# Kernel optimization log

Measured on AMD Instinct MI355X. Metric: run time of the kernel, lower is better.

Reference implementation:

```python
import jax, jax.numpy as jnp
import numpy as np

B, S, D, V = 2, 2048, 1024, 32000
EPS_LN = 1e-5
EPS_BN = 1e-5


def setup_inputs() -> dict:
    key = jax.random.key(0)
    ks = jax.random.split(key, 8)
    s = lambda k, shape: jax.random.normal(k, shape, jnp.float32) * 0.02
    return dict(
        X=jax.random.randint(ks[0], (B, S), 0, V, dtype=jnp.int32),
        emb=s(ks[1], (V, D)),
        w_hg=s(ks[2], (D, 2 * D)),            # minGRU to_hidden_and_gate (bias-free)
        conv_w=s(ks[3], (D, D, 3)),           # Conv1d OIW
        conv_b=jnp.zeros((D,), jnp.float32),
        bn_g=jnp.ones((D,), jnp.float32), bn_b=jnp.zeros((D,), jnp.float32),
        ln_g=jnp.ones((D,), jnp.float32), ln_b=jnp.zeros((D,), jnp.float32),
        w1=s(ks[4], (D, 2 * D)), b1=jnp.zeros((2 * D,), jnp.float32),
        w2=s(ks[5], (2 * D, 2 * D)), b2=jnp.zeros((2 * D,), jnp.float32),
        w3=s(ks[6], (2 * D, V)), b3=jnp.zeros((V,), jnp.float32),
    )


def _log_g(x):
    # log of g(x) = where(x>=0, x+0.5, sigmoid(x))
    return jnp.where(x >= 0, jnp.log(jax.nn.relu(x) + 0.5), -jax.nn.softplus(-x))


def _min_gru(x, w_hg):
    # Heinsen log-space associative scan (lucidrains minGRU, expansion=1)
    hg = x @ w_hg                              # [B,S,2D]
    hidden, gate = jnp.split(hg, 2, axis=-1)
    log_coeffs = -jax.nn.softplus(gate)        # log(1 - z)
    log_values = -jax.nn.softplus(-gate) + _log_g(hidden)  # log z + log h~
    a_star = jnp.cumsum(log_coeffs, axis=1)
    log_h = a_star + jax.lax.cumlogsumexp(log_values - a_star, axis=1)
    return jnp.exp(log_h)                      # [B,S,D]


def reference(X, emb, w_hg, conv_w, conv_b, bn_g, bn_b, ln_g, ln_b,
              w1, b1, w2, b2, w3, b3):
    x = emb[X]                                 # [B,S,D]
    shortcut = x
    h = _min_gru(x, w_hg)                      # dropout rate 0 -> identity
    mu = jnp.mean(h, axis=-1, keepdims=True)
    var = jnp.mean((h - mu) ** 2, axis=-1, keepdims=True)
    h = (h - mu) / jnp.sqrt(var + EPS_LN) * ln_g + ln_b
    x = h + shortcut
    xc = jnp.transpose(x, (0, 2, 1))           # [B,D,S]
    xc = jax.lax.conv_general_dilated(
        xc, conv_w, window_strides=(1,), padding=[(1, 1)],
        dimension_numbers=('NCW', 'OIW', 'NCW')) + conv_b[None, :, None]
    m = jnp.mean(xc, axis=(0, 2), keepdims=True)       # BN training-mode stats
    v = jnp.mean((xc - m) ** 2, axis=(0, 2), keepdims=True)
    xc = (xc - m) / jnp.sqrt(v + EPS_BN) * bn_g[None, :, None] + bn_b[None, :, None]
    x = jnp.transpose(xc, (0, 2, 1))           # [B,S,D]
    x = jax.nn.relu(x @ w1 + b1)
    x = jax.nn.relu(x @ w2 + b2)
    return x @ w3 + b3                         # [B,S,V]
```

## Files before the change

### kernel.cpp

```cpp
#include <hip/hip_runtime.h>
#include <hip/hip_bf16.h>

#define B_  2
#define S_  2048
#define D_  1024
#define V_  32000
#define BS_ 4096

typedef __attribute__((ext_vector_type(4))) float f32x4;
typedef __attribute__((ext_vector_type(8))) short short8;
typedef unsigned long long u64;
typedef unsigned short u16;

__device__ __forceinline__ u16 f2bf(float x) {
  unsigned int u = __float_as_uint(x);
  u += 0x7FFFu + ((u >> 16) & 1u);
  return (u16)(u >> 16);
}
__device__ __forceinline__ u64 pack4bf(float a, float b, float c, float d) {
  return (u64)f2bf(a) | ((u64)f2bf(b) << 16) | ((u64)f2bf(c) << 32) | ((u64)f2bf(d) << 48);
}

#define GLOAD_LDS16(g, l) __builtin_amdgcn_global_load_lds( \
    (const __attribute__((address_space(1))) void*)(g),     \
    (__attribute__((address_space(3))) void*)(l), 16, 0, 0)

__device__ __forceinline__ unsigned lds_addr32(const void* p) {
  return (unsigned)(uintptr_t)(const __attribute__((address_space(3))) void*)p;
}
__device__ __forceinline__ short8 ds_read128(unsigned a) {
  short8 r;
  asm volatile("ds_read_b128 %0, %1" : "=&v"(r) : "v"(a));
  return r;
}

template<bool RELU, bool BF16OUT, bool HASBIAS>
__global__ __launch_bounds__(256) void gemm_bt(
    const u16* __restrict__ A, const u16* __restrict__ Bt,
    const float* __restrict__ bias, void* __restrict__ Cout,
    int M, int N, int K)
{
  __shared__ __attribute__((aligned(16))) u16 Alds[128 * 64];
  __shared__ __attribute__((aligned(16))) u16 Blds[128 * 64];
  const int tid = threadIdx.x;
  const int w = tid >> 6, l = tid & 63;
  const int wr = w >> 1, wc = w & 1;
  const int m0 = blockIdx.y * 128, n0 = blockIdx.x * 128;
  const int lr = l >> 3, lc = l & 7;
  const int fr = l & 15, fq = l >> 4;

  const u16* Ag = A + (size_t)(m0 + w * 8 + lr) * K + lc * 8;
  const u16* Bg = Bt + (size_t)(n0 + w * 8 + lr) * K + lc * 8;

  f32x4 acc[4][4];
#pragma unroll
  for (int i = 0; i < 4; ++i)
#pragma unroll
    for (int j = 0; j < 4; ++j) acc[i][j] = {0.f, 0.f, 0.f, 0.f};

  for (int kt = 0; kt < K; kt += 64) {
#pragma unroll
    for (int r = 0; r < 4; ++r) {
      GLOAD_LDS16(Ag + (size_t)(r * 32) * K + kt, &Alds[(r * 32 + w * 8) * 64]);
      GLOAD_LDS16(Bg + (size_t)(r * 32) * K + kt, &Blds[(r * 32 + w * 8) * 64]);
    }
    __syncthreads();
#pragma unroll
    for (int ks = 0; ks < 2; ++ks) {
      short8 af[4], bfv[4];
#pragma unroll
      for (int i = 0; i < 4; ++i)
        af[i] = *reinterpret_cast<const short8*>(
            &Alds[(wr * 64 + i * 16 + fr) * 64 + ks * 32 + fq * 8]);
#pragma unroll
      for (int j = 0; j < 4; ++j)
        bfv[j] = *reinterpret_cast<const short8*>(
            &Blds[(wc * 64 + j * 16 + fr) * 64 + ks * 32 + fq * 8]);
#pragma unroll
      for (int i = 0; i < 4; ++i)
#pragma unroll
        for (int j = 0; j < 4; ++j)
          acc[i][j] = __builtin_amdgcn_mfma_f32_16x16x32_bf16(af[i], bfv[j], acc[i][j], 0, 0, 0);
    }
    __syncthreads();
  }

  const int row0 = m0 + wr * 64 + fq * 4;
  const int col0 = n0 + wc * 64 + fr;
#pragma unroll
  for (int j = 0; j < 4; ++j) {
    const int col = col0 + j * 16;
    const float bv = HASBIAS ? bias[col] : 0.f;
#pragma unroll
    for (int i = 0; i < 4; ++i) {
#pragma unroll
      for (int r = 0; r < 4; ++r) {
        const int row = row0 + i * 16 + r;
        float v = acc[i][j][r] + bv;
        if (RELU) v = fmaxf(v, 0.f);
        if (BF16OUT) ((u16*)Cout)[(size_t)row * N + col] = f2bf(v);
        else         ((float*)Cout)[(size_t)row * N + col] = v;
      }
    }
  }
}

#define BARRIER() __builtin_amdgcn_s_barrier()
#define WAITL0_PIN() do { asm volatile("s_waitcnt lgkmcnt(0)" ::: "memory"); \
                          __builtin_amdgcn_sched_barrier(0); } while (0)
#define VMCNTN(n) asm volatile("s_waitcnt vmcnt(" #n ")" ::: "memory")

template<bool RELU, bool BF16OUT, bool HASBIAS>
__global__ __launch_bounds__(512, 2) void gemm256_bt(
    const u16* __restrict__ A, const u16* __restrict__ Bt,
    const float* __restrict__ bias, void* __restrict__ Cout,
    int M, int N, int K)
{
  __shared__ __attribute__((aligned(16))) u16 LDS[65536];
  const int tid = threadIdx.x;
  const int w = tid >> 6, l = tid & 63;
  const int wr = w >> 2, wc = w & 3;
  const int fr = l & 15, fq = l >> 4;
  const unsigned ldsb = lds_addr32(&LDS[0]);

  const int MTt = M >> 8;
  const int total = MTt * (N >> 8);
  const int perx = total >> 3;
  const int p = (blockIdx.x & 7) * perx + (blockIdx.x >> 3);
  const int m0 = (p % MTt) << 8;
  const int n0 = (p / MTt) << 8;

  const int NT = K >> 6;
  const u16* Abase = A + (size_t)m0 * K;
  const u16* Bbase = Bt + (size_t)n0 * K;

  const int rq_[2] = { w * 16 + (l >> 3), w * 16 + 8 + (l >> 3) };
  const int gq_[2] = { (l & 7) ^ (rq_[0] & 7), (l & 7) ^ (rq_[1] & 7) };
  const u16* gA[2][2];
  const u16* gB[2][2];
#pragma unroll
  for (int h = 0; h < 2; ++h)
#pragma unroll
    for (int q = 0; q < 2; ++q) {
      gA[h][q] = Abase + (size_t)(h * 128 + rq_[q]) * K + gq_[q] * 8;
      gB[h][q] = Bbase + (size_t)(h * 128 + rq_[q]) * K + gq_[q] * 8;
    }

  const int swz0 = ((0 * 4 + fq) ^ (fr & 7)) * 16;
  const int swz1 = ((1 * 4 + fq) ^ (fr & 7)) * 16;
  const unsigned aB = ldsb + 16384u * wr + 128u * fr;
  const unsigned bB = ldsb + 32768u + 16384u * (wc >> 1) + 128u * ((wc & 1) * 64 + fr);
  const unsigned bA00 = aB + swz0,           bA01 = aB + swz1;
  const unsigned bA10 = aB + 65536u + swz0,  bA11 = aB + 65536u + swz1;
  const unsigned bB00 = bB + swz0,           bB01 = bB + swz1;
  const unsigned bB10 = bB + 65536u + swz0,  bB11 = bB + 65536u + swz1;

#define STAGE_A(h, t, buf) do { _Pragma("unroll")                            \
  for (int q_ = 0; q_ < 2; ++q_)                                             \
    GLOAD_LDS16(gA[h][q_] + (size_t)(t) * 64,                                \
                &LDS[(((buf) * 4) + (h)) * 8192 + (w * 128 + q_ * 64) * 8]); \
} while (0)
#define STAGE_B(h, t, buf) do { _Pragma("unroll")                            \
  for (int q_ = 0; q_ < 2; ++q_)                                             \
    GLOAD_LDS16(gB[h][q_] + (size_t)(t) * 64,                                \
                &LDS[(((buf) * 4) + 2 + (h)) * 8192 + (w * 128 + q_ * 64) * 8]); \
} while (0)

#define RDA_(arr, k0, k1, Q) do { _Pragma("unroll")                          \
  for (int i_ = 0; i_ < 4; ++i_) {                                           \
    arr[i_][0] = ds_read128((k0) + (Q) * 8192 + i_ * 2048);                  \
    arr[i_][1] = ds_read128((k1) + (Q) * 8192 + i_ * 2048);                  \
  } } while (0)
#define RDB_(arr, k0, k1, JQ) do { _Pragma("unroll")                         \
  for (int j_ = 0; j_ < 2; ++j_) {                                           \
    arr[j_][0] = ds_read128((k0) + (JQ) * 4096 + j_ * 2048);                 \
    arr[j_][1] = ds_read128((k1) + (JQ) * 4096 + j_ * 2048);                 \
  } } while (0)

#define MFMA_Q(arrA, arrB, itb, jtb) do { _Pragma("unroll")                  \
  for (int i_ = 0; i_ < 4; ++i_)                                             \
    _Pragma("unroll")                                                        \
    for (int j_ = 0; j_ < 2; ++j_)                                           \
      _Pragma("unroll")                                                      \
      for (int ks_ = 0; ks_ < 2; ++ks_)                                      \
        acc[(itb) + i_][(jtb) + j_] = __builtin_amdgcn_mfma_f32_16x16x32_bf16( \
            arrA[i_][ks_], arrB[j_][ks_], acc[(itb) + i_][(jtb) + j_], 0, 0, 0); \
} while (0)

  f32x4 acc[8][4];
#pragma unroll
  for (int i = 0; i < 8; ++i)
#pragma unroll
    for (int j = 0; j < 4; ++j) acc[i][j] = {0.f, 0.f, 0.f, 0.f};

  short8 a0[4][2], a1[4][2], b0[2][2], b1[2][2];

  STAGE_A(0, 0, 0); STAGE_A(1, 0, 0); STAGE_B(0, 0, 0); STAGE_B(1, 0, 0);
  STAGE_B(0, 1, 1); STAGE_A(0, 1, 1);
  VMCNTN(4);
  BARRIER();

#define TILE(t, cb, nb) do {                                                 \
                                         \
  RDA_(a0, bA##cb##0, bA##cb##1, 0);                                         \
  RDB_(b0, bB##cb##0, bB##cb##1, 0);                                         \
  if ((t) + 1 < NT) STAGE_A(1, (t) + 1, nb);                                 \
  BARRIER(); WAITL0_PIN();                                                   \
  __builtin_amdgcn_s_setprio(1); MFMA_Q(a0, b0, 0, 0); __builtin_amdgcn_s_setprio(0); \
  BARRIER();                                                                 \
                                            \
  RDB_(b1, bB##cb##0, bB##cb##1, 1);                                         \
  if ((t) + 1 < NT) STAGE_B(1, (t) + 1, nb);                                 \
  BARRIER(); WAITL0_PIN();                                                   \
  __builtin_amdgcn_s_setprio(1); MFMA_Q(a0, b1, 0, 2); __builtin_amdgcn_s_setprio(0); \
  BARRIER();                                                                 \
                                            \
  RDA_(a1, bA##cb##0, bA##cb##1, 1);                                         \
  if ((t) + 2 < NT) STAGE_B(0, (t) + 2, cb);                                 \
  BARRIER(); WAITL0_PIN();                                                   \
  __builtin_amdgcn_s_setprio(1); MFMA_Q(a1, b1, 4, 2); __builtin_amdgcn_s_setprio(0); \
  BARRIER();                                                                 \
                     \
  if ((t) + 2 < NT) STAGE_A(0, (t) + 2, cb);                                 \
  BARRIER(); WAITL0_PIN();                                                   \
  __builtin_amdgcn_s_setprio(1); MFMA_Q(a1, b0, 4, 0); __builtin_amdgcn_s_setprio(0); \
  if ((t) + 2 < NT) { VMCNTN(4); } else { VMCNTN(0); }                       \
  BARRIER();                                                                 \
} while (0)

  for (int t = 0; t < NT; t += 2) {
    TILE(t, 0, 1);
    TILE(t + 1, 1, 0);
  }
#undef TILE

  float* lf = (float*)(void*)(&LDS[0]) + (size_t)w * 1056;
  const int row_base = m0 + wr * 128;
  const int col_base = n0 + wc * 64;
  float bvv[4];
#pragma unroll
  for (int jt = 0; jt < 4; ++jt)
    bvv[jt] = HASBIAS ? bias[col_base + jt * 16 + fr] : 0.f;
  const int er = l >> 4, ec = (l & 15) * 4;
#pragma unroll
  for (int it = 0; it < 8; ++it) {
#pragma unroll
    for (int jt = 0; jt < 4; ++jt)
#pragma unroll
      for (int rr = 0; rr < 4; ++rr)
        lf[(fq * 4 + rr) * 66 + jt * 16 + fr] = acc[it][jt][rr] + bvv[jt];
#pragma unroll
    for (int ch = 0; ch < 4; ++ch) {
      f32x4 vv = *(const f32x4*)&lf[(ch * 4 + er) * 66 + ec];
      if (RELU) {
        vv[0] = fmaxf(vv[0], 0.f); vv[1] = fmaxf(vv[1], 0.f);
        vv[2] = fmaxf(vv[2], 0.f); vv[3] = fmaxf(vv[3], 0.f);
      }
      const int grow = row_base + it * 16 + ch * 4 + er;
      if (BF16OUT) {
        *(u64*)(&((u16*)Cout)[(size_t)grow * N + col_base + ec]) =
            pack4bf(vv[0], vv[1], vv[2], vv[3]);
      } else {
        *(f32x4*)(&((float*)Cout)[(size_t)grow * N + col_base + ec]) = vv;
      }
    }
  }
#undef STAGE_A
#undef STAGE_B
#undef RDA_
#undef RDB_
#undef MFMA_Q
}

__global__ __launch_bounds__(256) void transpose_f2b(
    const float* __restrict__ in, u16* __restrict__ out, int K, int N)
{
  __shared__ float t[32][33];
  const int n0 = blockIdx.x * 32, k0 = blockIdx.y * 32;
  const int r = threadIdx.x >> 5, cc = threadIdx.x & 31;
#pragma unroll
  for (int rr = 0; rr < 4; ++rr) {
    const int ki = rr * 8 + r;
    t[ki][cc] = in[(size_t)(k0 + ki) * N + n0 + cc];
  }
  __syncthreads();
#pragma unroll
  for (int rr = 0; rr < 4; ++rr) {
    const int ni = rr * 8 + r;
    out[(size_t)(n0 + ni) * K + k0 + cc] = f2bf(t[cc][ni]);
  }
}

__global__ __launch_bounds__(256) void convw_reorder(
    const float* __restrict__ cw, u16* __restrict__ out)
{
  const int gid = blockIdx.x * 256 + threadIdx.x;
  const int o = gid >> 10, i = gid & 1023;
  const float w0 = cw[(size_t)gid * 3 + 0];
  const float w1 = cw[(size_t)gid * 3 + 1];
  const float w2 = cw[(size_t)gid * 3 + 2];
  out[(size_t)o * 3072 + i]          = f2bf(w0);
  out[(size_t)o * 3072 + 1024 + i]   = f2bf(w1);
  out[(size_t)o * 3072 + 2048 + i]   = f2bf(w2);
}

__global__ __launch_bounds__(256) void gather_emb(
    const int* __restrict__ X, const float* __restrict__ emb, u16* __restrict__ xb)
{
  const int row = blockIdx.x;
  const int tok = X[row];
  const int d4 = threadIdx.x * 4;
  const float4 v = *reinterpret_cast<const float4*>(emb + (size_t)tok * D_ + d4);
  *(u64*)(&xb[(size_t)row * D_ + d4]) = pack4bf(v.x, v.y, v.z, v.w);
}

#define GRU_CP(hid_, gate_, h_, cp_) {                                   \
  const float t_ = __expf(-(gate_));                                     \
  const float z_ = 1.f / (1.f + t_);                                     \
  const float c_ = t_ * z_;                                              \
  const float g_ = ((hid_) >= 0.f) ? ((hid_) + 0.5f)                     \
                                   : (1.f / (1.f + __expf(-(hid_))));    \
  (h_) = c_ * (h_) + z_ * g_; (cp_) *= c_; }

#define GRU_NC(hid_, gate_, h_) {                                        \
  const float t_ = __expf(-(gate_));                                     \
  const float z_ = 1.f / (1.f + t_);                                     \
  const float g_ = ((hid_) >= 0.f) ? ((hid_) + 0.5f)                     \
                                   : (1.f / (1.f + __expf(-(hid_))));    \
  (h_) = (t_ * z_) * (h_) + z_ * g_; }

__global__ __launch_bounds__(256) void scan_partial(
    const float* __restrict__ hg, float* __restrict__ Cb, float* __restrict__ Vb)
{
  const int b = blockIdx.x >> 6, c = blockIdx.x & 63;
  const int d4 = threadIdx.x * 4;
  const float* base = hg + ((size_t)b * S_ + (size_t)c * 32) * (2 * D_);
  float h[4] = {0.f, 0.f, 0.f, 0.f}, cp[4] = {1.f, 1.f, 1.f, 1.f};
  for (int t = 0; t < 32; ++t) {
    const float4 hd = *reinterpret_cast<const float4*>(base + (size_t)t * (2 * D_) + d4);
    const float4 gt = *reinterpret_cast<const float4*>(base + (size_t)t * (2 * D_) + D_ + d4);
    GRU_CP(hd.x, gt.x, h[0], cp[0]); GRU_CP(hd.y, gt.y, h[1], cp[1]);
    GRU_CP(hd.z, gt.z, h[2], cp[2]); GRU_CP(hd.w, gt.w, h[3], cp[3]);
  }
  const size_t o = ((size_t)(b * 64 + c)) * D_ + d4;
  *(float4*)(Cb + o) = make_float4(cp[0], cp[1], cp[2], cp[3]);
  *(float4*)(Vb + o) = make_float4(h[0], h[1], h[2], h[3]);
}

__global__ void scan_carry(const float* __restrict__ Cb, const float* __restrict__ Vb,
                           float* __restrict__ Hs)
{
  const int gid = blockIdx.x * 256 + threadIdx.x;
  const int b = gid >> 10, d = gid & 1023;
  float h = 0.f;
  for (int c = 0; c < 64; ++c) {
    const size_t o = ((size_t)(b * 64 + c)) * D_ + d;
    Hs[o] = h;
    h = Cb[o] * h + Vb[o];
  }
}

__global__ __launch_bounds__(256) void scan_emit(
    const float* __restrict__ hg, const float* __restrict__ Hs,
    const int* __restrict__ X, const float* __restrict__ emb,
    const float* __restrict__ ln_g, const float* __restrict__ ln_b,
    u16* __restrict__ Aconv)
{
  __shared__ float red[4];
  const int b = blockIdx.x >> 6, c = blockIdx.x & 63;
  const int tid = threadIdx.x;
  const int w = tid >> 6, l = tid & 63;
  const int d4 = tid * 4;
  const float* base = hg + ((size_t)b * S_ + (size_t)c * 32) * (2 * D_);
  float h0, h1, h2, h3;
  {
    const float4 hs = *reinterpret_cast<const float4*>(Hs + ((size_t)(b * 64 + c)) * D_ + d4);
    h0 = hs.x; h1 = hs.y; h2 = hs.z; h3 = hs.w;
  }
  const float4 lg = *reinterpret_cast<const float4*>(ln_g + d4);
  const float4 lb = *reinterpret_cast<const float4*>(ln_b + d4);

  for (int t = 0; t < 32; ++t) {
    const int s = c * 32 + t;
    const float4 hd = *reinterpret_cast<const float4*>(base + (size_t)t * (2 * D_) + d4);
    const float4 gt = *reinterpret_cast<const float4*>(base + (size_t)t * (2 * D_) + D_ + d4);
    GRU_NC(hd.x, gt.x, h0); GRU_NC(hd.y, gt.y, h1);
    GRU_NC(hd.z, gt.z, h2); GRU_NC(hd.w, gt.w, h3);

    float sm = h0 + h1 + h2 + h3;
#pragma unroll
    for (int m = 1; m < 64; m <<= 1) sm += __shfl_xor(sm, m);
    __syncthreads();
    if (l == 0) red[w] = sm;
    __syncthreads();
    const float mu = (red[0] + red[1] + red[2] + red[3]) * (1.f / (float)D_);
    float q = (h0 - mu) * (h0 - mu) + (h1 - mu) * (h1 - mu) +
              (h2 - mu) * (h2 - mu) + (h3 - mu) * (h3 - mu);
#pragma unroll
    for (int m = 1; m < 64; m <<= 1) q += __shfl_xor(q, m);
    __syncthreads();
    if (l == 0) red[w] = q;
    __syncthreads();
    const float var = (red[0] + red[1] + red[2] + red[3]) * (1.f / (float)D_);
    const float rstd = rsqrtf(var + 1e-5f);

    const int tok = X[b * S_ + s];
    const float4 e = *reinterpret_cast<const float4*>(emb + (size_t)tok * D_ + d4);
    const float x0 = (h0 - mu) * rstd * lg.x + lb.x + e.x;
    const float x1 = (h1 - mu) * rstd * lg.y + lb.y + e.y;
    const float x2 = (h2 - mu) * rstd * lg.z + lb.z + e.z;
    const float x3 = (h3 - mu) * rstd * lg.w + lb.w + e.w;
    const u64 pk = pack4bf(x0, x1, x2, x3);

    const size_t row = (size_t)b * S_ + s;
    *(u64*)(&Aconv[row * 3072 + D_ + d4]) = pk;
    if (s + 1 < S_) *(u64*)(&Aconv[(row + 1) * 3072 + d4]) = pk;
    if (s > 0)      *(u64*)(&Aconv[(row - 1) * 3072 + 2 * D_ + d4]) = pk;
    if (s == 0)       *(u64*)(&Aconv[row * 3072 + d4]) = 0ull;
    if (s == S_ - 1)  *(u64*)(&Aconv[row * 3072 + 2 * D_ + d4]) = 0ull;
  }
}

__global__ __launch_bounds__(256) void bn_partial(
    const float* __restrict__ cv, float* __restrict__ ps, float* __restrict__ pq)
{
  const int blk = blockIdx.x;
  const int c4 = threadIdx.x * 4;
  float s0 = 0, s1 = 0, s2 = 0, s3 = 0, q0 = 0, q1 = 0, q2 = 0, q3 = 0;
  for (int r = 0; r < 64; ++r) {
    const float4 v = *reinterpret_cast<const float4*>(cv + ((size_t)blk * 64 + r) * D_ + c4);
    s0 += v.x; s1 += v.y; s2 += v.z; s3 += v.w;
    q0 += v.x * v.x; q1 += v.y * v.y; q2 += v.z * v.z; q3 += v.w * v.w;
  }
  *(float4*)(ps + (size_t)blk * D_ + c4) = make_float4(s0, s1, s2, s3);
  *(float4*)(pq + (size_t)blk * D_ + c4) = make_float4(q0, q1, q2, q3);
}

__global__ void bn_finalize(const float* __restrict__ ps, const float* __restrict__ pq,
                            const float* __restrict__ bn_g, const float* __restrict__ bn_b,
                            float* __restrict__ scale, float* __restrict__ shift)
{
  const int c = blockIdx.x * 256 + threadIdx.x;
  float s = 0.f, q = 0.f;
  for (int blk = 0; blk < 64; ++blk) { s += ps[(size_t)blk * D_ + c]; q += pq[(size_t)blk * D_ + c]; }
  const float m = s * (1.f / (float)BS_);
  const float var = q * (1.f / (float)BS_) - m * m;
  const float rs = rsqrtf(var + 1e-5f);
  const float sc = bn_g[c] * rs;
  scale[c] = sc;
  shift[c] = bn_b[c] - m * sc;
}

__global__ __launch_bounds__(256) void bn_apply(
    const float* __restrict__ cv, const float* __restrict__ scale,
    const float* __restrict__ shift, u16* __restrict__ out)
{
  const size_t idx = ((size_t)blockIdx.x * 256 + threadIdx.x) * 4;
  const int c = (int)(idx & 1023);
  const float4 v = *reinterpret_cast<const float4*>(cv + idx);
  const float4 sc = *reinterpret_cast<const float4*>(scale + c);
  const float4 sh = *reinterpret_cast<const float4*>(shift + c);
  *(u64*)(&out[idx]) = pack4bf(v.x * sc.x + sh.x, v.y * sc.y + sh.y,
                               v.z * sc.z + sh.z, v.w * sc.w + sh.w);
}

extern "C" void kernel_launch(void* const* d_in, const int* in_sizes, int n_in,
                              void* d_out, int out_size, void* d_ws, size_t ws_size,
                              hipStream_t stream)
{
  const int*   X      = (const int*)d_in[0];
  const float* emb    = (const float*)d_in[1];
  const float* w_hg   = (const float*)d_in[2];
  const float* conv_w = (const float*)d_in[3];
  const float* bn_g   = (const float*)d_in[5];
  const float* bn_b   = (const float*)d_in[6];
  const float* ln_g   = (const float*)d_in[7];
  const float* ln_b   = (const float*)d_in[8];
  const float* w1     = (const float*)d_in[9];
  const float* b1     = (const float*)d_in[10];
  const float* w2     = (const float*)d_in[11];
  const float* b2     = (const float*)d_in[12];
  const float* w3     = (const float*)d_in[13];
  const float* b3     = (const float*)d_in[14];
  float* out = (float*)d_out;
  char* ws = (char*)d_ws;

  const size_t OFF_A4    = 0;
  const size_t BASE      = 16777216;
  const size_t OFF_W3T   = BASE;
  const size_t OFF_WHGT  = BASE;
  const size_t OFF_W1T   = BASE + 4194304;
  const size_t OFF_W2T   = OFF_W1T + 4194304;
  const size_t OFF_WCVT  = OFF_W2T + 8388608;
  const size_t OFF_XBF   = OFF_WCVT + 6291456;
  const size_t OFF_HG    = OFF_XBF + 8388608;
  const size_t OFF_CB    = OFF_HG + 33554432;
  const size_t OFF_VB    = OFF_CB + 524288;
  const size_t OFF_HS    = OFF_VB + 524288;
  const size_t OFF_ACONV = OFF_HS + 524288;
  const size_t OFF_CVO   = OFF_ACONV + 25165824;
  const size_t OFF_A2    = OFF_CVO + 16777216;
  const size_t OFF_A3    = OFF_A2 + 8388608;
  const size_t OFF_BNS   = OFF_A3 + 16777216;
  const size_t OFF_BNQ   = OFF_BNS + 262144;
  const size_t OFF_SC    = OFF_BNQ + 262144;
  const size_t OFF_SH    = OFF_SC + 4096;
  (void)in_sizes; (void)n_in; (void)out_size; (void)ws_size;

  u16*   WHGT = (u16*)(ws + OFF_WHGT);
  u16*   W1T  = (u16*)(ws + OFF_W1T);
  u16*   W2T  = (u16*)(ws + OFF_W2T);
  u16*   W3T  = (u16*)(ws + OFF_W3T);
  u16*   WCVT = (u16*)(ws + OFF_WCVT);
  u16*   XBF  = (u16*)(ws + OFF_XBF);
  float* HG   = (float*)(ws + OFF_HG);
  float* CB   = (float*)(ws + OFF_CB);
  float* VB   = (float*)(ws + OFF_VB);
  float* HS   = (float*)(ws + OFF_HS);
  u16*   ACONV= (u16*)(ws + OFF_ACONV);
  float* CVO  = (float*)(ws + OFF_CVO);
  u16*   A2   = (u16*)(ws + OFF_A2);
  u16*   A3   = (u16*)(ws + OFF_A3);
  u16*   A4   = (u16*)(ws + OFF_A4);
  float* BNS  = (float*)(ws + OFF_BNS);
  float* BNQ  = (float*)(ws + OFF_BNQ);
  float* SC   = (float*)(ws + OFF_SC);
  float* SH   = (float*)(ws + OFF_SH);

  transpose_f2b<<<dim3(2048 / 32, 1024 / 32), 256, 0, stream>>>(w_hg, WHGT, 1024, 2048);
  transpose_f2b<<<dim3(2048 / 32, 1024 / 32), 256, 0, stream>>>(w1,   W1T,  1024, 2048);
  transpose_f2b<<<dim3(2048 / 32, 2048 / 32), 256, 0, stream>>>(w2,   W2T,  2048, 2048);
  convw_reorder<<<4096, 256, 0, stream>>>(conv_w, WCVT);

  gather_emb<<<BS_, 256, 0, stream>>>(X, emb, XBF);

  gemm_bt<false, false, false><<<dim3(2048 / 128, BS_ / 128), 256, 0, stream>>>(
      XBF, WHGT, nullptr, HG, BS_, 2048, 1024);

  scan_partial<<<B_ * 64, 256, 0, stream>>>(HG, CB, VB);
  scan_carry<<<8, 256, 0, stream>>>(CB, VB, HS);
  scan_emit<<<B_ * 64, 256, 0, stream>>>(HG, HS, X, emb, ln_g, ln_b, ACONV);

  gemm_bt<false, false, false><<<dim3(1024 / 128, BS_ / 128), 256, 0, stream>>>(
      ACONV, WCVT, nullptr, CVO, BS_, 1024, 3072);

  bn_partial<<<64, 256, 0, stream>>>(CVO, BNS, BNQ);
  bn_finalize<<<4, 256, 0, stream>>>(BNS, BNQ, bn_g, bn_b, SC, SH);
  bn_apply<<<4096, 256, 0, stream>>>(CVO, SC, SH, A2);

  gemm_bt<true, true, true><<<dim3(2048 / 128, BS_ / 128), 256, 0, stream>>>(
      A2, W1T, b1, A3, BS_, 2048, 1024);
  gemm_bt<true, true, true><<<dim3(2048 / 128, BS_ / 128), 256, 0, stream>>>(
      A3, W2T, b2, A4, BS_, 2048, 2048);

  transpose_f2b<<<dim3(V_ / 32, 2048 / 32), 256, 0, stream>>>(w3, W3T, 2048, V_);
  gemm256_bt<false, false, true><<<dim3((BS_ / 256) * (V_ / 256)), 512, 0, stream>>>(
      A4, W3T, b3, out, BS_, V_, 2048);
}
```

Baseline: 915.1 us.

## Switch vocab GEMM to 32x32x16 MFMA and chunked column-major tile order

```diff
diff --git a/kernel.cpp b/kernel.cpp
--- a/kernel.cpp
+++ b/kernel.cpp
@@ -8,6 +8,7 @@
 #define BS_ 4096
 
 typedef __attribute__((ext_vector_type(4))) float f32x4;
+typedef __attribute__((ext_vector_type(16))) float f32x16;
 typedef __attribute__((ext_vector_type(8))) short short8;
 typedef unsigned long long u64;
 typedef unsigned short u16;
@@ -27,11 +28,6 @@
 
 __device__ __forceinline__ unsigned lds_addr32(const void* p) {
   return (unsigned)(uintptr_t)(const __attribute__((address_space(3))) void*)p;
-}
-__device__ __forceinline__ short8 ds_read128(unsigned a) {
-  short8 r;
-  asm volatile("ds_read_b128 %0, %1" : "=&v"(r) : "v"(a));
-  return r;
 }
 
 template<bool RELU, bool BF16OUT, bool HASBIAS>
@@ -109,26 +105,27 @@
 #define WAITL0_PIN() do { asm volatile("s_waitcnt lgkmcnt(0)" ::: "memory"); \
                           __builtin_amdgcn_sched_barrier(0); } while (0)
 #define VMCNTN(n) asm volatile("s_waitcnt vmcnt(" #n ")" ::: "memory")
+#define DSR(dst, base, imm) \
+  asm volatile("ds_read_b128 %0, %1 offset:" #imm : "=&v"(dst) : "v"(base))
 
 template<bool RELU, bool BF16OUT, bool HASBIAS>
 __global__ __launch_bounds__(512, 2) void gemm256_bt(
     const u16* __restrict__ A, const u16* __restrict__ Bt,
     const float* __restrict__ bias, void* __restrict__ Cout,
-    int M, int N, int K)
+    int M, int N, int K, int CW)
 {
   __shared__ __attribute__((aligned(16))) u16 LDS[65536];
   const int tid = threadIdx.x;
   const int w = tid >> 6, l = tid & 63;
   const int wr = w >> 2, wc = w & 3;
-  const int fr = l & 15, fq = l >> 4;
+  const int hi = l >> 5, lo = l & 31;
   const unsigned ldsb = lds_addr32(&LDS[0]);
 
   const int MTt = M >> 8;
-  const int total = MTt * (N >> 8);
-  const int perx = total >> 3;
-  const int p = (blockIdx.x & 7) * perx + (blockIdx.x >> 3);
-  const int m0 = (p % MTt) << 8;
-  const int n0 = (p / MTt) << 8;
+  const int bpc = MTt * CW;
+  const int chunk = blockIdx.x / bpc, rem = blockIdx.x % bpc;
+  const int m0 = (rem % MTt) << 8;
+  const int n0 = ((chunk * CW) + rem / MTt) << 8;
 
   const int NT = K >> 6;
   const u16* Abase = A + (size_t)m0 * K;
@@ -146,14 +143,21 @@
       gB[h][q] = Bbase + (size_t)(h * 128 + rq_[q]) * K + gq_[q] * 8;
     }
 
-  const int swz0 = ((0 * 4 + fq) ^ (fr & 7)) * 16;
-  const int swz1 = ((1 * 4 + fq) ^ (fr & 7)) * 16;
-  const unsigned aB = ldsb + 16384u * wr + 128u * fr;
-  const unsigned bB = ldsb + 32768u + 16384u * (wc >> 1) + 128u * ((wc & 1) * 64 + fr);
-  const unsigned bA00 = aB + swz0,           bA01 = aB + swz1;
-  const unsigned bA10 = aB + 65536u + swz0,  bA11 = aB + 65536u + swz1;
-  const unsigned bB00 = bB + swz0,           bB01 = bB + swz1;
-  const unsigned bB10 = bB + 65536u + swz0,  bB11 = bB + 65536u + swz1;
+  unsigned swz[4];
+#pragma unroll
+  for (int s = 0; s < 4; ++s)
+    swz[s] = (unsigned)((((s * 2 + hi) ^ (l & 7))) * 16);
+  const unsigned baseA = ldsb + wr * 16384u + (unsigned)lo * 128u;
+  const unsigned baseB = ldsb + 32768u + (wc >> 1) * 16384u +
+                         (unsigned)((wc & 1) * 64 + lo) * 128u;
+  const unsigned bA00 = baseA + swz[0], bA01 = baseA + swz[1];
+  const unsigned bA02 = baseA + swz[2], bA03 = baseA + swz[3];
+  const unsigned bA10 = bA00 + 65536u, bA11 = bA01 + 65536u;
+  const unsigned bA12 = bA02 + 65536u, bA13 = bA03 + 65536u;
+  const unsigned bB00 = baseB + swz[0], bB01 = baseB + swz[1];
+  const unsigned bB02 = baseB + swz[2], bB03 = baseB + swz[3];
+  const unsigned bB10 = bB00 + 65536u, bB11 = bB01 + 65536u;
+  const unsigned bB12 = bB02 + 65536u, bB13 = bB03 + 65536u;
 
 #define STAGE_A(h, t, buf) do { _Pragma("unroll")                            \
   for (int q_ = 0; q_ < 2; ++q_)                                             \
@@ -166,34 +170,23 @@
                 &LDS[(((buf) * 4) + 2 + (h)) * 8192 + (w * 128 + q_ * 64) * 8]); \
 } while (0)
 
-#define RDA_(arr, k0, k1, Q) do { _Pragma("unroll")                          \
-  for (int i_ = 0; i_ < 4; ++i_) {                                           \
-    arr[i_][0] = ds_read128((k0) + (Q) * 8192 + i_ * 2048);                  \
-    arr[i_][1] = ds_read128((k1) + (Q) * 8192 + i_ * 2048);                  \
-  } } while (0)
-#define RDB_(arr, k0, k1, JQ) do { _Pragma("unroll")                         \
-  for (int j_ = 0; j_ < 2; ++j_) {                                           \
-    arr[j_][0] = ds_read128((k0) + (JQ) * 4096 + j_ * 2048);                 \
-    arr[j_][1] = ds_read128((k1) + (JQ) * 4096 + j_ * 2048);                 \
-  } } while (0)
-
-#define MFMA_Q(arrA, arrB, itb, jtb) do { _Pragma("unroll")                  \
-  for (int i_ = 0; i_ < 4; ++i_)                                             \
+#define MMQ2(IB, J, arrA, arrB) do { _Pragma("unroll")                       \
+  for (int ii_ = 0; ii_ < 2; ++ii_)                                          \
     _Pragma("unroll")                                                        \
-    for (int j_ = 0; j_ < 2; ++j_)                                           \
-      _Pragma("unroll")                                                      \
-      for (int ks_ = 0; ks_ < 2; ++ks_)                                      \
-        acc[(itb) + i_][(jtb) + j_] = __builtin_amdgcn_mfma_f32_16x16x32_bf16( \
-            arrA[i_][ks_], arrB[j_][ks_], acc[(itb) + i_][(jtb) + j_], 0, 0, 0); \
+    for (int s_ = 0; s_ < 4; ++s_)                                           \
+      acc[(IB) + ii_][J] = __builtin_amdgcn_mfma_f32_32x32x16_bf16(          \
+          arrA[ii_][s_], arrB[s_], acc[(IB) + ii_][J], 0, 0, 0);             \
 } while (0)
 
-  f32x4 acc[8][4];
-#pragma unroll
-  for (int i = 0; i < 8; ++i)
-#pragma unroll
-    for (int j = 0; j < 4; ++j) acc[i][j] = {0.f, 0.f, 0.f, 0.f};
-
-  short8 a0[4][2], a1[4][2], b0[2][2], b1[2][2];
+  f32x16 acc[4][2];
+#pragma unroll
+  for (int i = 0; i < 4; ++i)
+#pragma unroll
+    for (int j = 0; j < 2; ++j)
+#pragma unroll
+      for (int e = 0; e < 16; ++e) acc[i][j][e] = 0.f;
+
+  short8 a01[2][4], a23[2][4], b0[4], b1[4];
 
   STAGE_A(0, 0, 0); STAGE_A(1, 0, 0); STAGE_B(0, 0, 0); STAGE_B(1, 0, 0);
   STAGE_B(0, 1, 1); STAGE_A(0, 1, 1);
@@ -201,29 +194,37 @@
   BARRIER();
 
 #define TILE(t, cb, nb) do {                                                 \
-                                         \
-  RDA_(a0, bA##cb##0, bA##cb##1, 0);                                         \
-  RDB_(b0, bB##cb##0, bB##cb##1, 0);                                         \
+           \
+  DSR(a01[0][0], bA##cb##0, 0);    DSR(a01[0][1], bA##cb##1, 0);             \
+  DSR(a01[0][2], bA##cb##2, 0);    DSR(a01[0][3], bA##cb##3, 0);             \
+  DSR(a01[1][0], bA##cb##0, 4096); DSR(a01[1][1], bA##cb##1, 4096);          \
+  DSR(a01[1][2], bA##cb##2, 4096); DSR(a01[1][3], bA##cb##3, 4096);          \
+  DSR(b0[0], bB##cb##0, 0); DSR(b0[1], bB##cb##1, 0);                        \
+  DSR(b0[2], bB##cb##2, 0); DSR(b0[3], bB##cb##3, 0);                        \
   if ((t) + 1 < NT) STAGE_A(1, (t) + 1, nb);                                 \
   BARRIER(); WAITL0_PIN();                                                   \
-  __builtin_amdgcn_s_setprio(1); MFMA_Q(a0, b0, 0, 0); __builtin_amdgcn_s_setprio(0); \
+  __builtin_amdgcn_s_setprio(1); MMQ2(0, 0, a01, b0); __builtin_amdgcn_s_setprio(0); \
   BARRIER();                                                                 \
-                                            \
-  RDB_(b1, bB##cb##0, bB##cb##1, 1);                                         \
+                     \
+  DSR(b1[0], bB##cb##0, 4096); DSR(b1[1], bB##cb##1, 4096);                  \
+  DSR(b1[2], bB##cb##2, 4096); DSR(b1[3], bB##cb##3, 4096);                  \
   if ((t) + 1 < NT) STAGE_B(1, (t) + 1, nb);                                 \
   BARRIER(); WAITL0_PIN();                                                   \
-  __builtin_amdgcn_s_setprio(1); MFMA_Q(a0, b1, 0, 2); __builtin_amdgcn_s_setprio(0); \
+  __builtin_amdgcn_s_setprio(1); MMQ2(0, 1, a01, b1); __builtin_amdgcn_s_setprio(0); \
   BARRIER();                                                                 \
-                                            \
-  RDA_(a1, bA##cb##0, bA##cb##1, 1);                                         \
+                    \
+  DSR(a23[0][0], bA##cb##0, 8192);  DSR(a23[0][1], bA##cb##1, 8192);         \
+  DSR(a23[0][2], bA##cb##2, 8192);  DSR(a23[0][3], bA##cb##3, 8192);         \
+  DSR(a23[1][0], bA##cb##0, 12288); DSR(a23[1][1], bA##cb##1, 12288);        \
+  DSR(a23[1][2], bA##cb##2, 12288); DSR(a23[1][3], bA##cb##3, 12288);        \
   if ((t) + 2 < NT) STAGE_B(0, (t) + 2, cb);                                 \
   BARRIER(); WAITL0_PIN();                                                   \
-  __builtin_amdgcn_s_setprio(1); MFMA_Q(a1, b1, 4, 2); __builtin_amdgcn_s_setprio(0); \
+  __builtin_amdgcn_s_setprio(1); MMQ2(2, 1, a23, b1); __builtin_amdgcn_s_setprio(0); \
   BARRIER();                                                                 \
-                     \
+       \
   if ((t) + 2 < NT) STAGE_A(0, (t) + 2, cb);                                 \
   BARRIER(); WAITL0_PIN();                                                   \
-  __builtin_amdgcn_s_setprio(1); MFMA_Q(a1, b0, 4, 0); __builtin_amdgcn_s_setprio(0); \
+  __builtin_amdgcn_s_setprio(1); MMQ2(2, 0, a23, b0); __builtin_amdgcn_s_setprio(0); \
   if ((t) + 2 < NT) { VMCNTN(4); } else { VMCNTN(0); }                       \
   BARRIER();                                                                 \
 } while (0)
@@ -234,42 +235,41 @@
   }
 #undef TILE
 
-  float* lf = (float*)(void*)(&LDS[0]) + (size_t)w * 1056;
-  const int row_base = m0 + wr * 128;
-  const int col_base = n0 + wc * 64;
-  float bvv[4];
-#pragma unroll
-  for (int jt = 0; jt < 4; ++jt)
-    bvv[jt] = HASBIAS ? bias[col_base + jt * 16 + fr] : 0.f;
-  const int er = l >> 4, ec = (l & 15) * 4;
-#pragma unroll
-  for (int it = 0; it < 8; ++it) {
-#pragma unroll
-    for (int jt = 0; jt < 4; ++jt)
-#pragma unroll
-      for (int rr = 0; rr < 4; ++rr)
-        lf[(fq * 4 + rr) * 66 + jt * 16 + fr] = acc[it][jt][rr] + bvv[jt];
-#pragma unroll
-    for (int ch = 0; ch < 4; ++ch) {
-      f32x4 vv = *(const f32x4*)&lf[(ch * 4 + er) * 66 + ec];
-      if (RELU) {
-        vv[0] = fmaxf(vv[0], 0.f); vv[1] = fmaxf(vv[1], 0.f);
-        vv[2] = fmaxf(vv[2], 0.f); vv[3] = fmaxf(vv[3], 0.f);
+  float* lf = (float*)(void*)(&LDS[0]) + (size_t)w * 1152;
+  const int rowb = m0 + wr * 128;
+  const int colb = n0 + wc * 64;
+  float bvv[2];
+#pragma unroll
+  for (int j = 0; j < 2; ++j)
+    bvv[j] = HASBIAS ? bias[colb + j * 32 + lo] : 0.f;
+#pragma unroll
+  for (int i = 0; i < 4; ++i) {
+#pragma unroll
+    for (int j = 0; j < 2; ++j) {
+#pragma unroll
+      for (int reg = 0; reg < 16; ++reg) {
+        const int rowf = (reg & 3) + 8 * (reg >> 2) + 4 * hi;
+        float v = acc[i][j][reg] + bvv[j];
+        if (RELU) v = fmaxf(v, 0.f);
+        lf[rowf * 36 + lo] = v;
       }
-      const int grow = row_base + it * 16 + ch * 4 + er;
-      if (BF16OUT) {
-        *(u64*)(&((u16*)Cout)[(size_t)grow * N + col_base + ec]) =
-            pack4bf(vv[0], vv[1], vv[2], vv[3]);
-      } else {
-        *(f32x4*)(&((float*)Cout)[(size_t)grow * N + col_base + ec]) = vv;
+#pragma unroll
+      for (int rg = 0; rg < 4; ++rg) {
+        const f32x4 vv = *(const f32x4*)&lf[(rg * 8 + (l >> 3)) * 36 + (l & 7) * 4];
+        const int grow = rowb + i * 32 + rg * 8 + (l >> 3);
+        const int gcol = colb + j * 32 + (l & 7) * 4;
+        if (BF16OUT) {
+          *(u64*)(&((u16*)Cout)[(size_t)grow * N + gcol]) =
+              pack4bf(vv[0], vv[1], vv[2], vv[3]);
+        } else {
+          *(f32x4*)(&((float*)Cout)[(size_t)grow * N + gcol]) = vv;
+        }
       }
     }
   }
 #undef STAGE_A
 #undef STAGE_B
-#undef RDA_
-#undef RDB_
-#undef MFMA_Q
+#undef MMQ2
 }
 
 __global__ __launch_bounds__(256) void transpose_f2b(
@@ -555,5 +555,5 @@
 
   transpose_f2b<<<dim3(V_ / 32, 2048 / 32), 256, 0, stream>>>(w3, W3T, 2048, V_);
   gemm256_bt<false, false, true><<<dim3((BS_ / 256) * (V_ / 256)), 512, 0, stream>>>(
-      A4, W3T, b3, out, BS_, V_, 2048);
-}
+      A4, W3T, b3, out, BS_, V_, 2048, 16);
+}
```

New measurement: 932.7 us. No clear change (+1.9%).

## Restructure final GEMM tile pipeline into two phases and chunked block swizzle

Applied to the files above, without the earlier changes.

```diff
diff --git a/kernel.cpp b/kernel.cpp
--- a/kernel.cpp
+++ b/kernel.cpp
@@ -106,15 +106,15 @@
 }
 
 #define BARRIER() __builtin_amdgcn_s_barrier()
-#define WAITL0_PIN() do { asm volatile("s_waitcnt lgkmcnt(0)" ::: "memory"); \
-                          __builtin_amdgcn_sched_barrier(0); } while (0)
+#define LGKMN(n) do { asm volatile("s_waitcnt lgkmcnt(" #n ")" ::: "memory"); \
+                      __builtin_amdgcn_sched_barrier(0); } while (0)
 #define VMCNTN(n) asm volatile("s_waitcnt vmcnt(" #n ")" ::: "memory")
 
 template<bool RELU, bool BF16OUT, bool HASBIAS>
 __global__ __launch_bounds__(512, 2) void gemm256_bt(
     const u16* __restrict__ A, const u16* __restrict__ Bt,
     const float* __restrict__ bias, void* __restrict__ Cout,
-    int M, int N, int K)
+    int M, int N, int K, int CW)
 {
   __shared__ __attribute__((aligned(16))) u16 LDS[65536];
   const int tid = threadIdx.x;
@@ -124,11 +124,18 @@
   const unsigned ldsb = lds_addr32(&LDS[0]);
 
   const int MTt = M >> 8;
-  const int total = MTt * (N >> 8);
-  const int perx = total >> 3;
-  const int p = (blockIdx.x & 7) * perx + (blockIdx.x >> 3);
-  const int m0 = (p % MTt) << 8;
-  const int n0 = (p / MTt) << 8;
+  const int bpc = MTt * CW;
+  const int chunk = blockIdx.x / bpc, local = blockIdx.x % bpc;
+  int m_loc, n_loc;
+  if ((chunk + 1) * bpc <= MTt * (N >> 8)) {
+    n_loc = (local & 7) * 2 + ((local >> 3) & 1);
+    m_loc = local >> 4;
+  } else {
+    n_loc = local / MTt;
+    m_loc = local % MTt;
+  }
+  const int m0 = m_loc << 8;
+  const int n0 = (chunk * CW + n_loc) << 8;
 
   const int NT = K >> 6;
   const u16* Abase = A + (size_t)m0 * K;
@@ -201,29 +208,28 @@
   BARRIER();
 
 #define TILE(t, cb, nb) do {                                                 \
-                                         \
+     \
   RDA_(a0, bA##cb##0, bA##cb##1, 0);                                         \
   RDB_(b0, bB##cb##0, bB##cb##1, 0);                                         \
-  if ((t) + 1 < NT) STAGE_A(1, (t) + 1, nb);                                 \
-  BARRIER(); WAITL0_PIN();                                                   \
-  __builtin_amdgcn_s_setprio(1); MFMA_Q(a0, b0, 0, 0); __builtin_amdgcn_s_setprio(0); \
+  RDB_(b1, bB##cb##0, bB##cb##1, 1);                                         \
+  if ((t) + 1 < NT) { STAGE_A(1, (t) + 1, nb); STAGE_B(1, (t) + 1, nb); }    \
   BARRIER();                                                                 \
-                                            \
-  RDB_(b1, bB##cb##0, bB##cb##1, 1);                                         \
-  if ((t) + 1 < NT) STAGE_B(1, (t) + 1, nb);                                 \
-  BARRIER(); WAITL0_PIN();                                                   \
-  __builtin_amdgcn_s_setprio(1); MFMA_Q(a0, b1, 0, 2); __builtin_amdgcn_s_setprio(0); \
+  LGKMN(4);             \
+  __builtin_amdgcn_s_setprio(1);                                             \
+  MFMA_Q(a0, b0, 0, 0);                                                      \
+  LGKMN(0);                                                                  \
+  MFMA_Q(a0, b1, 0, 2);                                                      \
+  __builtin_amdgcn_s_setprio(0);                                             \
   BARRIER();                                                                 \
-                                            \
+                 \
   RDA_(a1, bA##cb##0, bA##cb##1, 1);                                         \
-  if ((t) + 2 < NT) STAGE_B(0, (t) + 2, cb);                                 \
-  BARRIER(); WAITL0_PIN();                                                   \
-  __builtin_amdgcn_s_setprio(1); MFMA_Q(a1, b1, 4, 2); __builtin_amdgcn_s_setprio(0); \
+  if ((t) + 2 < NT) { STAGE_B(0, (t) + 2, cb); STAGE_A(0, (t) + 2, cb); }    \
   BARRIER();                                                                 \
-                     \
-  if ((t) + 2 < NT) STAGE_A(0, (t) + 2, cb);                                 \
-  BARRIER(); WAITL0_PIN();                                                   \
-  __builtin_amdgcn_s_setprio(1); MFMA_Q(a1, b0, 4, 0); __builtin_amdgcn_s_setprio(0); \
+  LGKMN(0);                                                                  \
+  __builtin_amdgcn_s_setprio(1);                                             \
+  MFMA_Q(a1, b1, 4, 2);                                                      \
+  MFMA_Q(a1, b0, 4, 0);                                                      \
+  __builtin_amdgcn_s_setprio(0);                                             \
   if ((t) + 2 < NT) { VMCNTN(4); } else { VMCNTN(0); }                       \
   BARRIER();                                                                 \
 } while (0)
@@ -555,5 +561,5 @@
 
   transpose_f2b<<<dim3(V_ / 32, 2048 / 32), 256, 0, stream>>>(w3, W3T, 2048, V_);
   gemm256_bt<false, false, true><<<dim3((BS_ / 256) * (V_ / 256)), 512, 0, stream>>>(
-      A4, W3T, b3, out, BS_, V_, 2048);
-}
+      A4, W3T, b3, out, BS_, V_, 2048, 16);
+}
```

After: 901.0 us. About the same (-1.5%).
